# Kernel optimization log

Hardware: AMD Instinct MI355X
Metric: run time of the kernel (lower is better)

Reference implementation:

```python
import jax, jax.numpy as jnp
import numpy as np

N_NODES = 50000
N_EDGES = 800000
STATE_DIM = 16
EDGE_DIM = 8
OUT_DIM = 16
N_AGENTS = 320
B_GRAPHS = 64


def setup_inputs() -> dict:
    key = jax.random.key(0)
    ks = jax.random.split(key, 20)
    s = 0.1
    return {
        "x": jax.random.normal(ks[0], (N_NODES, STATE_DIM), dtype=jnp.float32),
        "edge_index": jax.random.randint(ks[1], (2, N_EDGES), 0, N_NODES, dtype=jnp.int64),
        "edge_attr": jax.random.normal(ks[2], (N_EDGES, EDGE_DIM), dtype=jnp.float32),
        "mask_idx": jax.random.randint(ks[3], (N_AGENTS,), 0, N_NODES, dtype=jnp.int64),
        "action": jax.random.normal(ks[4], (N_AGENTS,), dtype=jnp.float32),
        "B": B_GRAPHS,
        # NNConv edge MLP: Lin(edge_dim,16) -> ReLU -> Lin(16, state_dim*16)
        "w1": jax.random.normal(ks[5], (EDGE_DIM, 16), dtype=jnp.float32) * s,
        "b1": jnp.zeros((16,), dtype=jnp.float32),
        "w2": jax.random.normal(ks[6], (16, STATE_DIM * OUT_DIM), dtype=jnp.float32) * s,
        "b2": jnp.zeros((STATE_DIM * OUT_DIM,), dtype=jnp.float32),
        # NNConv root weight and bias
        "root": jax.random.normal(ks[7], (STATE_DIM, OUT_DIM), dtype=jnp.float32) * s,
        "bias": jnp.zeros((OUT_DIM,), dtype=jnp.float32),
        # trailing MLP: Lin(16+1,64) ELU Lin(64,64) ELU Lin(64,1)
        "fc1_w": jax.random.normal(ks[8], (OUT_DIM + 1, 64), dtype=jnp.float32) * s,
        "fc1_b": jnp.zeros((64,), dtype=jnp.float32),
        "fc2_w": jax.random.normal(ks[9], (64, 64), dtype=jnp.float32) * s,
        "fc2_b": jnp.zeros((64,), dtype=jnp.float32),
        "fc3_w": jax.random.normal(ks[10], (64, 1), dtype=jnp.float32) * s,
        "fc3_b": jnp.zeros((1,), dtype=jnp.float32),
    }


def reference(x, edge_index, edge_attr, mask_idx, action, B,
              w1, b1, w2, b2, root, bias,
              fc1_w, fc1_b, fc2_w, fc2_b, fc3_w, fc3_b):
    src, dst = edge_index[0], edge_index[1]
    # edge MLP -> per-edge transform matrices [E, state_dim, out_dim]
    h = jax.nn.relu(edge_attr @ w1 + b1)
    theta = (h @ w2 + b2).reshape(-1, STATE_DIM, OUT_DIM)
    # gather source features, per-edge matmul
    msg = jnp.einsum('ei,eio->eo', x[src], theta)  # [E, out_dim]
    # scatter-mean at destination
    summed = jax.ops.segment_sum(msg, dst, num_segments=N_NODES)
    deg = jax.ops.segment_sum(jnp.ones((msg.shape[0],), msg.dtype), dst, num_segments=N_NODES)
    aggr = summed / jnp.maximum(deg, 1.0)[:, None]
    out = aggr + x @ root + bias  # [N, out_dim]
    # select agent nodes, concat action, dense head
    xm = jnp.concatenate([out[mask_idx], action[:, None]], axis=-1)
    y = jax.nn.elu(xm @ fc1_w + fc1_b)
    y = jax.nn.elu(y @ fc2_w + fc2_b)
    y = y @ fc3_w + fc3_b
    return y.reshape(B, -1)
```

## Files before the change

### kernel.cpp

```cpp
#include <hip/hip_runtime.h>
#include <math.h>


#define NBM_WORDS 1568
#define QCAP      1024
#define AMAX      512

__global__ __launch_bounds__(256) void k_fused(
    const int* __restrict__ srcp, const int* __restrict__ dstp,
    const int4* __restrict__ dst4, int nquad, int E,
    const float* __restrict__ x, const float* __restrict__ edge_attr,
    const float* __restrict__ w1, const float* __restrict__ b1,
    const float* __restrict__ w2, const float* __restrict__ b2,
    const int* __restrict__ mask_idx, int A,
    float* __restrict__ aggr_c, int* __restrict__ deg_c) {
    __shared__ unsigned bm[NBM_WORDS];
    __shared__ float s_w2[4096];
    __shared__ float s_b2[256];
    __shared__ float s_w1[128];
    __shared__ float s_b1[16];
    __shared__ int   s_mask[AMAX];
    __shared__ int   s_qe[QCAP];
    __shared__ int   s_qd[QCAP];
    __shared__ int   s_qcnt;
    __shared__ float s_ea[16][8];
    __shared__ float s_x[16][16];
    __shared__ float s_h[16][16];
    __shared__ int   s_slot[16];

    int tid = threadIdx.x;
    if (tid == 0) s_qcnt = 0;
    for (int i = tid; i < NBM_WORDS; i += 256) bm[i] = 0u;
    for (int k = tid; k < 4096; k += 256) s_w2[k] = w2[k];
    s_b2[tid] = b2[tid];
    if (tid < 128) s_w1[tid] = w1[tid];
    if (tid < 16)  s_b1[tid] = b1[tid];
    __syncthreads();
    for (int a = tid; a < A; a += 256) {
        int node = mask_idx[a];
        s_mask[a] = node;
        atomicOr(&bm[node >> 5], 1u << (node & 31));
    }
    __syncthreads();

    int q = blockIdx.x * 256 + tid;
    if (q < nquad) {
        int4 d = dst4[q];
        int e0 = q * 4;
        if ((bm[d.x >> 5] >> (d.x & 31)) & 1) { int p = atomicAdd(&s_qcnt, 1); if (p < QCAP) { s_qe[p] = e0;     s_qd[p] = d.x; } }
        if ((bm[d.y >> 5] >> (d.y & 31)) & 1) { int p = atomicAdd(&s_qcnt, 1); if (p < QCAP) { s_qe[p] = e0 + 1; s_qd[p] = d.y; } }
        if ((bm[d.z >> 5] >> (d.z & 31)) & 1) { int p = atomicAdd(&s_qcnt, 1); if (p < QCAP) { s_qe[p] = e0 + 2; s_qd[p] = d.z; } }
        if ((bm[d.w >> 5] >> (d.w & 31)) & 1) { int p = atomicAdd(&s_qcnt, 1); if (p < QCAP) { s_qe[p] = e0 + 3; s_qd[p] = d.w; } }
    }
    if (blockIdx.x == 0 && tid == 0) {
        for (int e = nquad * 4; e < E; ++e) {
            int dn = dstp[e];
            if ((bm[dn >> 5] >> (dn & 31)) & 1) {
                int p = atomicAdd(&s_qcnt, 1);
                if (p < QCAP) { s_qe[p] = e; s_qd[p] = dn; }
            }
        }
    }
    __syncthreads();
    int nq = s_qcnt; if (nq > QCAP) nq = QCAP;
    if (nq == 0) return;

    int el = tid >> 4;
    int o  = tid & 15;
    for (int base = 0; base < nq; base += 16) {
        int idx = base + el;
        bool valid = (idx < nq);
        int e = valid ? s_qe[idx] : -1;
        if (o == 0) s_slot[el] = 0x7fffffff;
        __syncthreads();
        if (valid) {
            int dn = s_qd[idx];
            int best = 0x7fffffff;
            for (int a = o; a < A; a += 16)
                if (s_mask[a] == dn && a < best) best = a;
            if (best != 0x7fffffff) atomicMin(&s_slot[el], best);
            if (o < 8) s_ea[el][o] = edge_attr[(long)e * 8 + o];
            s_x[el][o] = x[(long)srcp[e] * 16 + o];
        }
        __syncthreads();
        if (valid) {
            if (o == 0) atomicAdd(&deg_c[s_slot[el]], 1);
            float hj = s_b1[o];
            #pragma unroll
            for (int k = 0; k < 8; ++k) hj += s_ea[el][k] * s_w1[k * 16 + o];
            s_h[el][o] = hj > 0.f ? hj : 0.f;
        }
        __syncthreads();
        if (valid) {
            float hr[16], xr[16];
            #pragma unroll
            for (int j = 0; j < 16; ++j) hr[j] = s_h[el][j];
            #pragma unroll
            for (int i = 0; i < 16; ++i) xr[i] = s_x[el][i];
            float m = 0.f;
            #pragma unroll
            for (int i = 0; i < 16; ++i) {
                float tacc = s_b2[i * 16 + o];
                #pragma unroll
                for (int j = 0; j < 16; ++j) tacc += hr[j] * s_w2[j * 256 + i * 16 + o];
                m += xr[i] * tacc;
            }
            atomicAdd(&aggr_c[s_slot[el] * 16 + o], m);
        }
        __syncthreads();
    }
}

__global__ __launch_bounds__(64) void k_head(
    const int* __restrict__ mask_idx, int A, const float* __restrict__ action,
    const float* __restrict__ x,
    const float* __restrict__ aggr_c, const int* __restrict__ deg_c,
    const float* __restrict__ root, const float* __restrict__ bias,
    const float* __restrict__ fc1_w, const float* __restrict__ fc1_b,
    const float* __restrict__ fc2_w, const float* __restrict__ fc2_b,
    const float* __restrict__ fc3_w, const float* __restrict__ fc3_b,
    float* __restrict__ out) {
    __shared__ float xm[17];
    __shared__ float y1[64];
    int a = blockIdx.x;
    int t = threadIdx.x;
    int node = mask_idx[a];
    int best = 0x7fffffff;
    for (int i = t; i < A; i += 64)
        if (mask_idx[i] == node && i < best) best = i;
    #pragma unroll
    for (int off = 32; off > 0; off >>= 1) {
        int o2 = __shfl_xor(best, off, 64);
        if (o2 < best) best = o2;
    }
    int s = best;
    if (t < 16) {
        float r = bias[t];
        #pragma unroll
        for (int i = 0; i < 16; ++i) r += x[(long)node * 16 + i] * root[i * 16 + t];
        float dg = (float)deg_c[s];
        if (dg < 1.f) dg = 1.f;
        xm[t] = aggr_c[s * 16 + t] / dg + r;
    } else if (t == 16) {
        xm[16] = action[a];
    }
    __syncthreads();
    float v = fc1_b[t];
    #pragma unroll
    for (int k = 0; k < 17; ++k) v += xm[k] * fc1_w[k * 64 + t];
    v = v > 0.f ? v : expm1f(v);
    y1[t] = v;
    __syncthreads();
    float u = fc2_b[t];
    #pragma unroll
    for (int j = 0; j < 64; ++j) u += y1[j] * fc2_w[j * 64 + t];
    u = u > 0.f ? u : expm1f(u);
    float p = u * fc3_w[t];
    #pragma unroll
    for (int off = 32; off > 0; off >>= 1) p += __shfl_down(p, off, 64);
    if (t == 0) out[a] = p + fc3_b[0];
}

extern "C" void kernel_launch(void* const* d_in, const int* in_sizes, int n_in,
                              void* d_out, int out_size, void* d_ws, size_t ws_size,
                              hipStream_t stream) {
    const float* x      = (const float*)d_in[0];
    const int*   ei     = (const int*)  d_in[1];
    const float* ea     = (const float*)d_in[2];
    const int*   mask   = (const int*)  d_in[3];
    const float* action = (const float*)d_in[4];
    const float* w1     = (const float*)d_in[6];
    const float* b1     = (const float*)d_in[7];
    const float* w2     = (const float*)d_in[8];
    const float* b2     = (const float*)d_in[9];
    const float* root   = (const float*)d_in[10];
    const float* bias   = (const float*)d_in[11];
    const float* fc1_w  = (const float*)d_in[12];
    const float* fc1_b  = (const float*)d_in[13];
    const float* fc2_w  = (const float*)d_in[14];
    const float* fc2_b  = (const float*)d_in[15];
    const float* fc3_w  = (const float*)d_in[16];
    const float* fc3_b  = (const float*)d_in[17];

    const int E = in_sizes[2] / 8;
    const int A = in_sizes[4];

    const int* srcp = ei;
    const int* dstp = ei + E;

    float* aggr  = (float*)d_ws;
    int*   deg_c = (int*)(aggr + (size_t)A * 16);
    size_t fixed_bytes = (size_t)A * 16 * 4 + (size_t)A * 4;

    const int nquad = E / 4;
    const int nblocks = (nquad + 255) / 256;

    hipMemsetAsync(d_ws, 0, fixed_bytes, stream);
    k_fused<<<nblocks, 256, 0, stream>>>(srcp, dstp, (const int4*)dstp, nquad, E,
                                         x, ea, w1, b1, w2, b2, mask, A, aggr, deg_c);
    k_head<<<A, 64, 0, stream>>>(mask, A, action, x, aggr, deg_c,
                                 root, bias, fc1_w, fc1_b, fc2_w, fc2_b, fc3_w, fc3_b,
                                 (float*)d_out);
}
```

Baseline: 123.6 us.

## Replace bitmap and linear slot search with shared hash table, fewer blocks

Swaps the per-block node bitmap and the per-edge linear scan over the agent list for a shared-memory open-addressing hash table that maps node to its lowest agent slot. Matched edges are queued as a single packed word (edge << 9 | slot), which removes the slot search and one barrier from the edge-processing loop. Each block now covers 1024 quads instead of 256, so setup (weight loads, table build) is amortized over four times as many edges, at the cost of fewer blocks in flight. The packing assumes fewer than 512 agents and edge ids below 2^23, and the queue write no longer checks capacity.

Result: slower. 133.0 us (+7.7%).

```diff
diff --git a/kernel.cpp b/kernel.cpp
--- a/kernel.cpp
+++ b/kernel.cpp
@@ -2,9 +2,11 @@
 #include <math.h>
 
 
-#define NBM_WORDS 1568
-#define QCAP      1024
-#define AMAX      512
+#define HASH_SZ   2048
+#define HASH_MASK 2047
+#define HEMPTY    0xFFFFFFFFu
+#define QUADS_PB  1024
+#define QCAP      4096
 
 __global__ __launch_bounds__(256) void k_fused(
     const int* __restrict__ srcp, const int* __restrict__ dstp,
@@ -14,53 +16,68 @@
     const float* __restrict__ w2, const float* __restrict__ b2,
     const int* __restrict__ mask_idx, int A,
     float* __restrict__ aggr_c, int* __restrict__ deg_c) {
-    __shared__ unsigned bm[NBM_WORDS];
+    __shared__ unsigned s_hash[HASH_SZ];
     __shared__ float s_w2[4096];
     __shared__ float s_b2[256];
     __shared__ float s_w1[128];
     __shared__ float s_b1[16];
-    __shared__ int   s_mask[AMAX];
-    __shared__ int   s_qe[QCAP];
-    __shared__ int   s_qd[QCAP];
+    __shared__ unsigned s_q[QCAP];
     __shared__ int   s_qcnt;
     __shared__ float s_ea[16][8];
     __shared__ float s_x[16][16];
     __shared__ float s_h[16][16];
-    __shared__ int   s_slot[16];
 
     int tid = threadIdx.x;
     if (tid == 0) s_qcnt = 0;
-    for (int i = tid; i < NBM_WORDS; i += 256) bm[i] = 0u;
+    #pragma unroll
+    for (int i = tid; i < HASH_SZ; i += 256) s_hash[i] = HEMPTY;
     for (int k = tid; k < 4096; k += 256) s_w2[k] = w2[k];
     s_b2[tid] = b2[tid];
     if (tid < 128) s_w1[tid] = w1[tid];
     if (tid < 16)  s_b1[tid] = b1[tid];
     __syncthreads();
+
     for (int a = tid; a < A; a += 256) {
         int node = mask_idx[a];
-        s_mask[a] = node;
-        atomicOr(&bm[node >> 5], 1u << (node & 31));
-    }
-    __syncthreads();
-
-    int q = blockIdx.x * 256 + tid;
-    if (q < nquad) {
-        int4 d = dst4[q];
-        int e0 = q * 4;
-        if ((bm[d.x >> 5] >> (d.x & 31)) & 1) { int p = atomicAdd(&s_qcnt, 1); if (p < QCAP) { s_qe[p] = e0;     s_qd[p] = d.x; } }
-        if ((bm[d.y >> 5] >> (d.y & 31)) & 1) { int p = atomicAdd(&s_qcnt, 1); if (p < QCAP) { s_qe[p] = e0 + 1; s_qd[p] = d.y; } }
-        if ((bm[d.z >> 5] >> (d.z & 31)) & 1) { int p = atomicAdd(&s_qcnt, 1); if (p < QCAP) { s_qe[p] = e0 + 2; s_qd[p] = d.z; } }
-        if ((bm[d.w >> 5] >> (d.w & 31)) & 1) { int p = atomicAdd(&s_qcnt, 1); if (p < QCAP) { s_qe[p] = e0 + 3; s_qd[p] = d.w; } }
-    }
-    if (blockIdx.x == 0 && tid == 0) {
-        for (int e = nquad * 4; e < E; ++e) {
-            int dn = dstp[e];
-            if ((bm[dn >> 5] >> (dn & 31)) & 1) {
+        unsigned pk = ((unsigned)node << 9) | (unsigned)a;
+        unsigned h = ((unsigned)node * 2654435761u) >> 21;
+        for (;;) {
+            unsigned cur = atomicCAS(&s_hash[h], HEMPTY, pk);
+            if (cur == HEMPTY) break;
+            if ((cur >> 9) == (unsigned)node) { atomicMin(&s_hash[h], pk); break; }
+            h = (h + 1) & HASH_MASK;
+        }
+    }
+    __syncthreads();
+
+    auto probe = [&](int node, int e) {
+        unsigned h = ((unsigned)node * 2654435761u) >> 21;
+        for (;;) {
+            unsigned cur = s_hash[h];
+            if (cur == HEMPTY) return;
+            if ((cur >> 9) == (unsigned)node) {
                 int p = atomicAdd(&s_qcnt, 1);
-                if (p < QCAP) { s_qe[p] = e; s_qd[p] = dn; }
+                s_q[p] = ((unsigned)e << 9) | (cur & 511u);
+                return;
             }
-        }
-    }
+            h = (h + 1) & HASH_MASK;
+        }
+    };
+    int q0 = blockIdx.x * QUADS_PB;
+    #pragma unroll
+    for (int it = 0; it < 4; ++it) {
+        int q = q0 + it * 256 + tid;
+        if (q < nquad) {
+            int4 d = dst4[q];
+            int e0 = q * 4;
+            probe(d.x, e0);
+            probe(d.y, e0 + 1);
+            probe(d.z, e0 + 2);
+            probe(d.w, e0 + 3);
+        }
+    }
+    if (blockIdx.x == 0 && tid == 0)
+        for (int e = nquad * 4; e < E; ++e) probe(dstp[e], e);
     __syncthreads();
     int nq = s_qcnt; if (nq > QCAP) nq = QCAP;
     if (nq == 0) return;
@@ -70,21 +87,16 @@
     for (int base = 0; base < nq; base += 16) {
         int idx = base + el;
         bool valid = (idx < nq);
-        int e = valid ? s_qe[idx] : -1;
-        if (o == 0) s_slot[el] = 0x7fffffff;
+        int e = 0, slot = 0;
+        if (valid) {
+            unsigned pk = s_q[idx];
+            e = (int)(pk >> 9);
+            slot = (int)(pk & 511u);
+            if (o < 8) s_ea[el][o] = edge_attr[(long)e * 8 + o];
+            s_x[el][o] = x[(long)srcp[e] * 16 + o];
+        }
         __syncthreads();
         if (valid) {
-            int dn = s_qd[idx];
-            int best = 0x7fffffff;
-            for (int a = o; a < A; a += 16)
-                if (s_mask[a] == dn && a < best) best = a;
-            if (best != 0x7fffffff) atomicMin(&s_slot[el], best);
-            if (o < 8) s_ea[el][o] = edge_attr[(long)e * 8 + o];
-            s_x[el][o] = x[(long)srcp[e] * 16 + o];
-        }
-        __syncthreads();
-        if (valid) {
-            if (o == 0) atomicAdd(&deg_c[s_slot[el]], 1);
             float hj = s_b1[o];
             #pragma unroll
             for (int k = 0; k < 8; ++k) hj += s_ea[el][k] * s_w1[k * 16 + o];
@@ -105,7 +117,8 @@
                 for (int j = 0; j < 16; ++j) tacc += hr[j] * s_w2[j * 256 + i * 16 + o];
                 m += xr[i] * tacc;
             }
-            atomicAdd(&aggr_c[s_slot[el] * 16 + o], m);
+            atomicAdd(&aggr_c[slot * 16 + o], m);
+            if (o == 0) atomicAdd(&deg_c[slot], 1);
         }
         __syncthreads();
     }
@@ -193,7 +206,7 @@
     size_t fixed_bytes = (size_t)A * 16 * 4 + (size_t)A * 4;
 
     const int nquad = E / 4;
-    const int nblocks = (nquad + 255) / 256;
+    const int nblocks = (nquad + QUADS_PB - 1) / QUADS_PB;
 
     hipMemsetAsync(d_ws, 0, fixed_bytes, stream);
     k_fused<<<nblocks, 256, 0, stream>>>(srcp, dstp, (const int4*)dstp, nquad, E,
```
